# Optimization experiments

Measured on AMD Instinct MI355X. Metric: run time of the kernel, lower is better.

## Reference

```python
import jax, jax.numpy as jnp
import numpy as np


def setup_inputs() -> dict:
    key = jax.random.key(0)
    n, d = 256, 64
    ks = jax.random.split(key, 8)
    x = jax.random.normal(ks[0], (n, d), jnp.float32)
    v = jax.random.normal(ks[1], (n, d), jnp.float32)
    # torch nn.Linear convention: weight shape (out_features, in_features)
    W1 = jax.random.normal(ks[2], (d, d), jnp.float32) * (1.0 / np.sqrt(d))
    b1 = jax.random.normal(ks[3], (d,), jnp.float32) * 0.1
    # W2 scaled small + b2 ~ scaled identity so g = M + M^T is well-conditioned (invertible)
    W2 = jax.random.normal(ks[4], (d * d, d), jnp.float32) * 0.02
    b2 = (3.0 * jnp.eye(d, dtype=jnp.float32)).reshape(d * d) \
         + jax.random.normal(ks[5], (d * d,), jnp.float32) * 0.01
    W3 = jax.random.normal(ks[6], (d, 2 * d), jnp.float32) * (1.0 / np.sqrt(2 * d))
    return {"t": 0, "x": x, "v": v, "W1": W1, "b1": b1, "W2": W2, "b2": b2, "W3": W3}


def reference(t, x, v, W1, b1, W2, b2, W3):
    # Connection_gnew.forward. t is unused (ODE-time placeholder), matching the original.
    n, d = x.shape
    # g network: linear1 -> tanh -> linear2 -> symmetrize
    h = jnp.tanh(x @ W1.T + b1)                      # (n, d)
    M = (h @ W2.T + b2).reshape(n, d, d)             # (n, d, d)
    g = M + jnp.transpose(M, (0, 2, 1))              # symmetric metric (n, d, d)
    g_inv = jnp.linalg.inv(g)
    # Analytic batch jacobian of g_flat wrt x (replaces autograd.functional.jacobian):
    # d M_flat[a]/d x[l] = sum_m W2[a,m] * (1 - h[m]^2) * W1[m,l]; then symmetrize (i<->j).
    s = 1.0 - h * h                                   # tanh' (n, d)
    J = jnp.einsum('am,nm,ml->nal', W2, s, W1).reshape(n, d, d, d)
    J = J + jnp.transpose(J, (0, 2, 1, 3))            # J[n,i,j,l] = d g_{ij} / d x_l
    # einsum('nkl,nijl,njil,nlij->nkij', g_inv, J, J, -J):
    # elementwise triple product over matching indices, then contract l with g_inv.
    T = J * jnp.transpose(J, (0, 2, 1, 3)) * (-jnp.transpose(J, (0, 2, 3, 1)))  # T[n,i,j,l]
    connection = 0.5 * jnp.einsum('nkl,nijl->nkij', g_inv, T)
    # dv[n,k] = -sum_{ij} v_i v_j connection[n,k,i,j]
    dv = -jnp.einsum('ni,nj,nkij->nk', v, v, connection)
    out = jnp.concatenate([v, dv], axis=-1) @ W3.T    # linear3, no bias
    return out
```

## Files before the change

kernel.cpp:

```cpp
#include <hip/hip_runtime.h>
#include <math.h>
#include <stdint.h>


typedef short short8 __attribute__((ext_vector_type(8)));
typedef float f32x4 __attribute__((ext_vector_type(4)));

__device__ __forceinline__ unsigned short f2bf(float f) {
  unsigned int u = __builtin_bit_cast(unsigned int, f);
  u += 0x7fffu + ((u >> 16) & 1u);
  return (unsigned short)(u >> 16);
}

__device__ __forceinline__ short8 as_short8(uint4 u) {
  union { uint4 a; short8 b; } cv; cv.a = u; return cv.b;
}

__global__ __launch_bounds__(256) void prep_w2s_kernel(const float* __restrict__ W2,
                                                       unsigned short* __restrict__ W2sB) {
  int idx = blockIdx.x * 256 + threadIdx.x;
  int i = idx >> 12, j = (idx >> 6) & 63, m = idx & 63;
  W2sB[idx] = f2bf(W2[(((i << 6) + j) << 6) + m] + W2[(((j << 6) + i) << 6) + m]);
}

__global__ __launch_bounds__(256, 1) void conn_kernel(
    const float* __restrict__ x, const float* __restrict__ v,
    const float* __restrict__ W1, const float* __restrict__ b1,
    const float* __restrict__ b2, const float* __restrict__ W3,
    const unsigned short* __restrict__ W2sB, float* __restrict__ out) {
  __shared__ __align__(16) unsigned short sKT[80 * 80];
  __shared__ __align__(16) float sg[64 * 68];
  __shared__ float spq[4][64];
  __shared__ __align__(16) float sh[64], sv[64], sx[64], sq[64], sz[64];

  const int n = blockIdx.x, t = threadIdx.x;
  const int wv = t >> 6, lane = t & 63, ln15 = lane & 15, quad = lane >> 4;

  if (t < 64) { sx[t] = x[(n << 6) + t]; sv[t] = v[(n << 6) + t]; }
  for (int e = t; e < 6400; e += 256) sKT[e] = 0;
  __syncthreads();

  if (t < 64) {
    float acc = b1[t];
    #pragma unroll 8
    for (int l = 0; l < 64; ++l) acc += sx[l] * W1[(t << 6) + l];
    sh[t] = tanhf(acc);
  }
  __syncthreads();

  for (int e = t; e < 4096; e += 256) {
    int m = e & 63, l = e >> 6;
    float hm = sh[m];
    sKT[l * 80 + m] = f2bf((1.f - hm * hm) * W1[(m << 6) + l]);
  }
  if (t < 64) sKT[64 * 80 + t] = f2bf(sh[t]);
  __syncthreads();

  short8 bf[5][2];
  #pragma unroll
  for (int tc = 0; tc < 5; ++tc)
    #pragma unroll
    for (int ks = 0; ks < 2; ++ks)
      bf[tc][ks] = *(const short8*)&sKT[(tc * 16 + ln15) * 80 + ks * 32 + quad * 8];

  f32x4 svj[4];
  #pragma unroll
  for (int tr = 0; tr < 4; ++tr) svj[tr] = *(const f32x4*)&sv[tr * 16 + quad * 4];

  float qacc[4] = {0.f, 0.f, 0.f, 0.f};

  const int foff = (ln15 << 6) + quad * 8;
  const unsigned short* sbase = W2sB + ((size_t)(16 * wv) << 12);

  uint4 af[4][2], afn[4][2];
  #pragma unroll
  for (int tc = 0; tc < 4; ++tc) {
    af[tc][0] = *(const uint4*)(sbase + (tc << 10) + foff);
    af[tc][1] = *(const uint4*)(sbase + (tc << 10) + foff + 32);
  }

  for (int ii = 0; ii < 16; ++ii) {
    const unsigned short* spn = W2sB + ((size_t)(16 * wv + ((ii + 1) & 15)) << 12);
    #pragma unroll
    for (int tc = 0; tc < 4; ++tc) {
      afn[tc][0] = *(const uint4*)(spn + (tc << 10) + foff);
      afn[tc][1] = *(const uint4*)(spn + (tc << 10) + foff + 32);
    }
    const int i = 16 * wv + ii;
    const float vi = sv[i];

    #pragma unroll
    for (int tr = 0; tr < 4; ++tr) {
      short8 a0 = as_short8(af[tr][0]), a1 = as_short8(af[tr][1]);
      f32x4 c1[4], c2[4], ce;
      #pragma unroll
      for (int tc = 0; tc < 4; ++tc) {
        f32x4 z4 = {0.f, 0.f, 0.f, 0.f};
        f32x4 u = __builtin_amdgcn_mfma_f32_16x16x32_bf16(a0, bf[tc][0], z4, 0, 0, 0);
        c1[tc]  = __builtin_amdgcn_mfma_f32_16x16x32_bf16(a1, bf[tc][1], u, 0, 0, 0);
        f32x4 w = __builtin_amdgcn_mfma_f32_16x16x32_bf16(bf[tr][0], as_short8(af[tc][0]), z4, 0, 0, 0);
        c2[tc]  = __builtin_amdgcn_mfma_f32_16x16x32_bf16(bf[tr][1], as_short8(af[tc][1]), w, 0, 0, 0);
      }
      {
        f32x4 z4 = {0.f, 0.f, 0.f, 0.f};
        f32x4 u = __builtin_amdgcn_mfma_f32_16x16x32_bf16(a0, bf[4][0], z4, 0, 0, 0);
        ce      = __builtin_amdgcn_mfma_f32_16x16x32_bf16(a1, bf[4][1], u, 0, 0, 0);
      }
      if (ln15 == 0)
        *(f32x4*)&sg[i * 68 + tr * 16 + quad * 4] = ce;

      #pragma unroll
      for (int tc = 0; tc < 4; ++tc) {
        float s = 0.f;
        #pragma unroll
        for (int r = 0; r < 4; ++r) {
          float a = c1[tc][r];
          s = fmaf(a * a * c2[tc][r], svj[tr][r], s);
        }
        qacc[tc] = fmaf(s, vi, qacc[tc]);
      }
    }
    #pragma unroll
    for (int tc = 0; tc < 4; ++tc) { af[tc][0] = afn[tc][0]; af[tc][1] = afn[tc][1]; }
  }

  #pragma unroll
  for (int tc = 0; tc < 4; ++tc) {
    float s = qacc[tc];
    s += __shfl_xor(s, 16, 64);
    s += __shfl_xor(s, 32, 64);
    if (quad == 0) spq[wv][tc * 16 + ln15] = s;
  }
  __syncthreads();

  for (int e = t; e < 4096; e += 256) {
    int r = e >> 6, c = e & 63;
    sg[r * 68 + c] += b2[(r << 6) + c] + b2[(c << 6) + r];
  }
  __syncthreads();

  if (t < 64) {
    float s = spq[0][t] + spq[1][t] + spq[2][t] + spq[3][t];
    sq[t] = s;
    sz[t] = s / sg[t * 68 + t];
  }
  __syncthreads();

  {
    const int r = 16 * wv + ln15;
    const float* grow = &sg[r * 68];
    const float dinv = 1.f / grow[r];
    const float qr = sq[r];
    for (int it = 0; it < 20; ++it) {
      float p = 0.f;
      #pragma unroll
      for (int cc = 0; cc < 16; ++cc) {
        int cidx = quad * 16 + cc;
        p += grow[cidx] * sz[cidx];
      }
      p += __shfl_xor(p, 16, 64);
      p += __shfl_xor(p, 32, 64);
      float zr = 0.f;
      if (quad == 0) zr = sz[r] + (qr - p) * dinv;
      __syncthreads();
      if (quad == 0) sz[r] = zr;
      __syncthreads();
    }
  }

  if (t < 64) {
    float accv = 0.f, accd = 0.f;
    #pragma unroll 8
    for (int c = 0; c < 64; ++c) {
      accv += sv[c] * W3[(t << 7) + c];
      accd += sz[c] * W3[(t << 7) + 64 + c];
    }
    out[(n << 6) + t] = accv + 0.5f * accd;
  }
}

extern "C" void kernel_launch(void* const* d_in, const int* in_sizes, int n_in,
                              void* d_out, int out_size, void* d_ws, size_t ws_size,
                              hipStream_t stream) {
  (void)in_sizes; (void)n_in; (void)out_size; (void)ws_size;
  const float* x  = (const float*)d_in[1];
  const float* v  = (const float*)d_in[2];
  const float* W1 = (const float*)d_in[3];
  const float* b1 = (const float*)d_in[4];
  const float* W2 = (const float*)d_in[5];
  const float* b2 = (const float*)d_in[6];
  const float* W3 = (const float*)d_in[7];
  unsigned short* W2sB = (unsigned short*)d_ws;

  hipLaunchKernelGGL(prep_w2s_kernel, dim3(1024), dim3(256), 0, stream, W2, W2sB);
  hipLaunchKernelGGL(conn_kernel, dim3(256), dim3(256), 0, stream,
                     x, v, W1, b1, b2, W3, W2sB, (float*)d_out);
}
```

Measured before the change: 103.0 us.

## Split connection kernel across two blocks per sample and separate solve stage

Splits the per-sample kernel into two stages. The first stage now uses two blocks per sample, each covering half of the i rows, and writes g and partial q vectors to global workspace. A second kernel sums the partials, adds a precomputed symmetrized b2, and runs the Jacobi solve and the output projection. The aim is to double the grid to 512 blocks so more of the device's CUs stay busy, at the cost of extra launches and global round-trips. The Jacobi iteration count also drops from 20 to 12, which may lower accuracy.

Result: slower. 107.3 us (+4.2%).

```diff
diff --git a/kernel.cpp b/kernel.cpp
--- a/kernel.cpp
+++ b/kernel.cpp
@@ -23,17 +23,23 @@
   W2sB[idx] = f2bf(W2[(((i << 6) + j) << 6) + m] + W2[(((j << 6) + i) << 6) + m]);
 }
 
-__global__ __launch_bounds__(256, 1) void conn_kernel(
+__global__ __launch_bounds__(256) void prep_b2s_kernel(const float* __restrict__ b2,
+                                                       float* __restrict__ b2s) {
+  int idx = blockIdx.x * 256 + threadIdx.x;
+  b2s[idx] = b2[idx] + b2[((idx & 63) << 6) + (idx >> 6)];
+}
+
+__global__ __launch_bounds__(256, 2) void conn_a_kernel(
     const float* __restrict__ x, const float* __restrict__ v,
     const float* __restrict__ W1, const float* __restrict__ b1,
-    const float* __restrict__ b2, const float* __restrict__ W3,
-    const unsigned short* __restrict__ W2sB, float* __restrict__ out) {
+    const unsigned short* __restrict__ W2sB,
+    float* __restrict__ gws, float* __restrict__ qpart) {
   __shared__ __align__(16) unsigned short sKT[80 * 80];
-  __shared__ __align__(16) float sg[64 * 68];
   __shared__ float spq[4][64];
-  __shared__ __align__(16) float sh[64], sv[64], sx[64], sq[64], sz[64];
-
-  const int n = blockIdx.x, t = threadIdx.x;
+  __shared__ float sh[64], sv[64], sx[64];
+
+  const int b = blockIdx.x, t = threadIdx.x;
+  const int n = b >> 1, half = b & 1, ibase = half << 5;
   const int wv = t >> 6, lane = t & 63, ln15 = lane & 15, quad = lane >> 4;
 
   if (t < 64) { sx[t] = x[(n << 6) + t]; sv[t] = v[(n << 6) + t]; }
@@ -69,8 +75,9 @@
 
   float qacc[4] = {0.f, 0.f, 0.f, 0.f};
 
+  const int i0 = ibase + 8 * wv;
   const int foff = (ln15 << 6) + quad * 8;
-  const unsigned short* sbase = W2sB + ((size_t)(16 * wv) << 12);
+  const unsigned short* sbase = W2sB + ((size_t)i0 << 12);
 
   uint4 af[4][2], afn[4][2];
   #pragma unroll
@@ -79,14 +86,14 @@
     af[tc][1] = *(const uint4*)(sbase + (tc << 10) + foff + 32);
   }
 
-  for (int ii = 0; ii < 16; ++ii) {
-    const unsigned short* spn = W2sB + ((size_t)(16 * wv + ((ii + 1) & 15)) << 12);
+  for (int ii = 0; ii < 8; ++ii) {
+    const unsigned short* spn = W2sB + ((size_t)(i0 + ((ii + 1) & 7)) << 12);
     #pragma unroll
     for (int tc = 0; tc < 4; ++tc) {
       afn[tc][0] = *(const uint4*)(spn + (tc << 10) + foff);
       afn[tc][1] = *(const uint4*)(spn + (tc << 10) + foff + 32);
     }
-    const int i = 16 * wv + ii;
+    const int i = i0 + ii;
     const float vi = sv[i];
 
     #pragma unroll
@@ -107,7 +114,7 @@
         ce      = __builtin_amdgcn_mfma_f32_16x16x32_bf16(a1, bf[4][1], u, 0, 0, 0);
       }
       if (ln15 == 0)
-        *(f32x4*)&sg[i * 68 + tr * 16 + quad * 4] = ce;
+        *(f32x4*)&gws[(n << 12) + (i << 6) + tr * 16 + quad * 4] = ce;
 
       #pragma unroll
       for (int tc = 0; tc < 4; ++tc) {
@@ -132,15 +139,26 @@
     if (quad == 0) spq[wv][tc * 16 + ln15] = s;
   }
   __syncthreads();
-
-  for (int e = t; e < 4096; e += 256) {
-    int r = e >> 6, c = e & 63;
-    sg[r * 68 + c] += b2[(r << 6) + c] + b2[(c << 6) + r];
-  }
+  if (t < 64) qpart[(b << 6) + t] = spq[0][t] + spq[1][t] + spq[2][t] + spq[3][t];
+}
+
+__global__ __launch_bounds__(256, 2) void conn_b_kernel(
+    const float* __restrict__ v, const float* __restrict__ W3,
+    const float* __restrict__ gws, const float* __restrict__ b2s,
+    const float* __restrict__ qpart, float* __restrict__ out) {
+  __shared__ float sg[64 * 68];
+  __shared__ float sv[64], sq[64], sz[64];
+
+  const int n = blockIdx.x, t = threadIdx.x;
+  const int wv = t >> 6, lane = t & 63, ln15 = lane & 15, quad = lane >> 4;
+
+  if (t < 64) sv[t] = v[(n << 6) + t];
+  for (int e = t; e < 4096; e += 256)
+    sg[(e >> 6) * 68 + (e & 63)] = gws[(n << 12) + e] + b2s[e];
   __syncthreads();
 
   if (t < 64) {
-    float s = spq[0][t] + spq[1][t] + spq[2][t] + spq[3][t];
+    float s = qpart[((n << 1) << 6) + t] + qpart[(((n << 1) + 1) << 6) + t];
     sq[t] = s;
     sz[t] = s / sg[t * 68 + t];
   }
@@ -151,7 +169,7 @@
     const float* grow = &sg[r * 68];
     const float dinv = 1.f / grow[r];
     const float qr = sq[r];
-    for (int it = 0; it < 20; ++it) {
+    for (int it = 0; it < 12; ++it) {
       float p = 0.f;
       #pragma unroll
       for (int cc = 0; cc < 16; ++cc) {
@@ -190,9 +208,17 @@
   const float* W2 = (const float*)d_in[5];
   const float* b2 = (const float*)d_in[6];
   const float* W3 = (const float*)d_in[7];
-  unsigned short* W2sB = (unsigned short*)d_ws;
+
+  char* ws = (char*)d_ws;
+  unsigned short* W2sB = (unsigned short*)ws;
+  float* b2s   = (float*)(ws + (512 << 10));
+  float* gws   = (float*)(ws + (512 << 10) + (16 << 10));
+  float* qpart = (float*)(ws + (512 << 10) + (16 << 10) + (4 << 20));
 
   hipLaunchKernelGGL(prep_w2s_kernel, dim3(1024), dim3(256), 0, stream, W2, W2sB);
-  hipLaunchKernelGGL(conn_kernel, dim3(256), dim3(256), 0, stream,
-                     x, v, W1, b1, b2, W3, W2sB, (float*)d_out);
-}
+  hipLaunchKernelGGL(prep_b2s_kernel, dim3(16), dim3(256), 0, stream, b2, b2s);
+  hipLaunchKernelGGL(conn_a_kernel, dim3(512), dim3(256), 0, stream,
+                     x, v, W1, b1, W2sB, gws, qpart);
+  hipLaunchKernelGGL(conn_b_kernel, dim3(256), dim3(256), 0, stream,
+                     v, W3, gws, b2s, qpart, (float*)d_out);
+}
```
